# Performance work log

Measured on AMD Instinct MI355X. Metric: run time of the kernel, lower is better.

Reference implementation:

```python
import jax, jax.numpy as jnp
import numpy as np

B, X, Y, Z, C = 1, 16, 16, 16, 768
NUM_HEADS = 12


def setup_inputs() -> dict:
    key = jax.random.key(0)
    k0, k1, k2 = jax.random.split(key, 3)
    x = jax.random.normal(k0, (B, X, Y, Z, C), dtype=jnp.float32)
    # Linear weights stored as [in, out] (torch stores [out, in]; math is x @ W_in_out + b)
    w_qkv = jax.random.normal(k1, (C, 3 * C), dtype=jnp.float32) * 0.02
    b_qkv = jnp.zeros((3 * C,), dtype=jnp.float32)
    w_proj = jax.random.normal(k2, (C, C), dtype=jnp.float32) * 0.02
    b_proj = jnp.zeros((C,), dtype=jnp.float32)
    return {"x": x, "w_qkv": w_qkv, "b_qkv": b_qkv, "w_proj": w_proj, "b_proj": b_proj}


def reference(x, w_qkv, b_qkv, w_proj, b_proj):
    b, xx, yy, zz, c = x.shape
    h = NUM_HEADS
    hd = c // h
    scale = hd ** (-0.5)
    n = xx * yy * zz  # flatten 3D grid into tokens

    qkv = x.reshape(b, n, c) @ w_qkv + b_qkv          # [B, N, 3C]
    qkv = qkv.reshape(b, n, 3, h, hd).transpose(2, 0, 3, 1, 4)  # [3, B, H, N, hd]
    q, k, v = qkv[0], qkv[1], qkv[2]

    attn = jnp.einsum('bhnd,bhmd->bhnm', q * scale, k)  # [B, H, N, N]
    attn = jax.nn.softmax(attn, axis=-1)
    out = jnp.einsum('bhnm,bhmd->bhnd', attn, v)        # [B, H, N, hd]
    out = out.transpose(0, 2, 1, 3).reshape(b, n, c)
    out = out @ w_proj + b_proj
    return out.reshape(b, xx, yy, zz, c)
```

## Files before the change

### kernel.cpp

```cpp
#include <hip/hip_runtime.h>
#include <cstddef>

#define N_TOK 4096
#define C_DIM 768
#define H_NUM 12
#define C3    2304
#define NSPLIT 4

typedef unsigned short u16;
using short8  = __attribute__((ext_vector_type(8))) short;
using floatx4 = __attribute__((ext_vector_type(4))) float;
using u16x4   = __attribute__((ext_vector_type(4))) u16;
using uint4v  = __attribute__((ext_vector_type(4))) unsigned;

#define K2SCALE 0.18033688011112043f

__device__ __forceinline__ u16 f2bf(float f) {
  union { float f; unsigned u; } v; v.f = f;
  unsigned r = v.u + 0x7FFFu + ((v.u >> 16) & 1u);
  return (u16)(r >> 16);
}

__device__ __forceinline__ unsigned permpack(float a, float b) {
  union { float f; unsigned u; } x, y; x.f = a; y.f = b;
  return __builtin_amdgcn_perm(y.u, x.u, 0x07060302u);
}

__device__ __forceinline__ float aexp2(float x) {
  float r;
  asm("v_exp_f32 %0, %1" : "=v"(r) : "v"(x));
  return r;
}

__device__ __forceinline__ float arcp(float x) {
  float r;
  asm("v_rcp_f32 %0, %1" : "=v"(r) : "v"(x));
  return r;
}

__device__ __forceinline__ void pl_swap32(unsigned &a, unsigned &b) {
#if __has_builtin(__builtin_amdgcn_permlane32_swap)
  auto r = __builtin_amdgcn_permlane32_swap(a, b, false, false);
  a = r[0]; b = r[1];
#else
  asm("v_permlane32_swap_b32 %0, %1" : "+v"(a), "+v"(b));
#endif
}
__device__ __forceinline__ void pl_swap16(unsigned &a, unsigned &b) {
#if __has_builtin(__builtin_amdgcn_permlane16_swap)
  auto r = __builtin_amdgcn_permlane16_swap(a, b, false, false);
  a = r[0]; b = r[1];
#else
  asm("v_permlane16_swap_b32 %0, %1" : "+v"(a), "+v"(b));
#endif
}

__device__ __forceinline__ void gload_lds16(const void* g, void* l) {
  __builtin_amdgcn_global_load_lds(
      (const __attribute__((address_space(1))) unsigned int*)g,
      (__attribute__((address_space(3))) unsigned int*)l, 16, 0, 0);
}

__global__ void k_pre(const float* __restrict__ x, u16* __restrict__ xb,
                      const float* __restrict__ wq, u16* __restrict__ wqT,
                      const float* __restrict__ wp, u16* __restrict__ wpT,
                      float* __restrict__ Oz) {
  __shared__ float tile[32][33];
  const int b = blockIdx.x;
  if (b >= 5376) {
    size_t i = (size_t)(b - 5376) * 256 + threadIdx.x;
    float4 z; z.x = 0.f; z.y = 0.f; z.z = 0.f; z.w = 0.f;
    ((float4*)Oz)[i] = z;
    return;
  }
  if (b < 3072) {
    int i = b * 256 + threadIdx.x;
    float4 f = ((const float4*)x)[i];
    u16x4 o;
    o[0] = f2bf(f.x); o[1] = f2bf(f.y); o[2] = f2bf(f.z); o[3] = f2bf(f.w);
    ((u16x4*)xb)[i] = o;
    return;
  }
  const float* in; u16* out; int Cc, bx, by;
  if (b < 4800) { int t = b - 3072; in = wq; out = wqT; Cc = 2304; bx = t % 72; by = t / 72; }
  else          { int t = b - 4800; in = wp; out = wpT; Cc = 768;  bx = t % 24; by = t / 24; }
  const int R = 768;
  const int tx = threadIdx.x & 31;
  const int ty = threadIdx.x >> 5;
  const int c0 = bx * 32, r0 = by * 32;
#pragma unroll
  for (int i = 0; i < 32; i += 8)
    tile[ty + i][tx] = in[(size_t)(r0 + ty + i) * Cc + c0 + tx];
  __syncthreads();
#pragma unroll
  for (int i = 0; i < 32; i += 8)
    out[(size_t)(c0 + ty + i) * R + r0 + tx] = f2bf(tile[tx][ty + i]);
}

template <int MODE>
__global__ __launch_bounds__(256)
void k_gemm_bt(const u16* __restrict__ A, const u16* __restrict__ B,
               const float* __restrict__ bias, void* __restrict__ outp,
               u16* __restrict__ vT, int K) {
  __shared__ u16 As[128 * 32];
  __shared__ u16 Bs[128 * 32];
  const int tid  = threadIdx.x;
  const int wave = tid >> 6, lane = tid & 63, quad = lane >> 4, l16 = lane & 15;
  const int wrow = wave >> 1, wcol = wave & 1;
  const int bm = blockIdx.y, bn = blockIdx.x;
  const int r3 = l16 & 3;

  floatx4 acc[4][4];
#pragma unroll
  for (int i = 0; i < 4; ++i)
#pragma unroll
    for (int j = 0; j < 4; ++j)
#pragma unroll
      for (int r = 0; r < 4; ++r) acc[i][j][r] = 0.f;

  const int ar = tid >> 2;
  const int ac = ((tid & 3) ^ (ar & 3)) * 8;
  const u16* gA = A + (size_t)(bm * 128 + ar) * K + ac;
  const u16* gB = B + (size_t)(bn * 128 + ar) * K + ac;
  u16* lA = &As[0] + tid * 8;
  u16* lB = &Bs[0] + tid * 8;

  for (int k0 = 0; k0 < K; k0 += 32) {
    gload_lds16(gA + k0,                  lA);
    gload_lds16(gA + k0 + (size_t)64 * K, lA + 2048);
    gload_lds16(gB + k0,                  lB);
    gload_lds16(gB + k0 + (size_t)64 * K, lB + 2048);
    __syncthreads();
    short8 af[4], bf[4];
#pragma unroll
    for (int t = 0; t < 4; ++t) {
      af[t] = *(const short8*)&As[(wrow * 64 + t * 16 + l16) * 32 + ((quad ^ r3) * 8)];
      bf[t] = *(const short8*)&Bs[(wcol * 64 + t * 16 + l16) * 32 + ((quad ^ r3) * 8)];
    }
#pragma unroll
    for (int tm = 0; tm < 4; ++tm)
#pragma unroll
      for (int tn = 0; tn < 4; ++tn)
        acc[tm][tn] = __builtin_amdgcn_mfma_f32_16x16x32_bf16(af[tm], bf[tn], acc[tm][tn], 0, 0, 0);
    __syncthreads();
  }

  if (MODE == 0) {
    u16* qkv = (u16*)outp;
    const float qs = (bn < 6) ? K2SCALE : 1.0f;
#pragma unroll
    for (int tn = 0; tn < 4; ++tn) {
      const int col = bn * 128 + wcol * 64 + tn * 16 + l16;
      const float bc = bias[col];
      if (col < 1536) {
#pragma unroll
        for (int tm = 0; tm < 4; ++tm) {
          const int rowb = bm * 128 + wrow * 64 + tm * 16 + quad * 4;
#pragma unroll
          for (int r = 0; r < 4; ++r)
            qkv[(size_t)(rowb + r) * C3 + col] = f2bf((acc[tm][tn][r] + bc) * qs);
        }
      } else {
        const int hd_ = col - 1536;
#pragma unroll
        for (int tm = 0; tm < 4; ++tm) {
          const int rowb = bm * 128 + wrow * 64 + tm * 16 + quad * 4;
          u16x4 pk;
#pragma unroll
          for (int r = 0; r < 4; ++r) pk[r] = f2bf(acc[tm][tn][r] + bc);
          *(u16x4*)&vT[(size_t)hd_ * N_TOK + rowb] = pk;
        }
      }
    }
  } else {
    float* out = (float*)outp;
#pragma unroll
    for (int tn = 0; tn < 4; ++tn) {
      const int col = bn * 128 + wcol * 64 + tn * 16 + l16;
      const float bc = bias[col];
#pragma unroll
      for (int tm = 0; tm < 4; ++tm) {
        const int rowb = bm * 128 + wrow * 64 + tm * 16 + quad * 4;
#pragma unroll
        for (int r = 0; r < 4; ++r)
          out[(size_t)(rowb + r) * C_DIM + col] = acc[tm][tn][r] + bc;
      }
    }
  }
}

__global__ __launch_bounds__(256, 4)
void k_flash(const u16* __restrict__ qkv, const u16* __restrict__ vT,
             float* __restrict__ Opart, float* __restrict__ lpart) {
  __shared__ u16 Ks[2][64 * 64];
  __shared__ u16 Vs[2][64 * 64];
  const int tid  = threadIdx.x;
  const int wave = tid >> 6, lane = tid & 63, quad = lane >> 4, l16 = lane & 15;
  const int qt = blockIdx.x, h = blockIdx.y, split = blockIdx.z;
  const int lr = tid >> 3;
  const int lc = ((tid & 7) ^ (lr & 7)) * 8;
  const int r7 = l16 & 7;
  const int kb = split * 1024;

  short8 bq[2][2];
#pragma unroll
  for (int qs = 0; qs < 2; ++qs)
#pragma unroll
    for (int ks = 0; ks < 2; ++ks)
      bq[qs][ks] = *(const short8*)&qkv[(size_t)(qt * 128 + wave * 32 + qs * 16 + l16) * C3
                                        + h * 64 + ks * 32 + quad * 8];

  const u16* gk = qkv + (size_t)lr * C3 + C_DIM + h * 64 + lc;
  const u16* gv = vT + (size_t)(h * 64 + lr) * N_TOK + lc;

  auto stage = [&](int b, int m0) {
#pragma unroll
    for (int p = 0; p < 2; ++p) {
      gload_lds16(gk + (size_t)(m0 + p * 32) * C3,    &Ks[b][p * 2048 + tid * 8]);
      gload_lds16(gv + (size_t)(p * 32) * N_TOK + m0, &Vs[b][p * 2048 + tid * 8]);
    }
  };

  floatx4 o0[4], o1[4], l0, l1, zv;
#pragma unroll
  for (int r = 0; r < 4; ++r) { zv[r] = 0.f; l0[r] = 0.f; l1[r] = 0.f; }
#pragma unroll
  for (int d = 0; d < 4; ++d)
#pragma unroll
    for (int r = 0; r < 4; ++r) { o0[d][r] = 0.f; o1[d][r] = 0.f; }

  short8 ones;
#pragma unroll
  for (int i = 0; i < 8; ++i) ones[i] = (short)0x3F80;

  auto compute = [&](int b) __attribute__((always_inline)) {
    const u16* kbp = &Ks[b][0];
    const u16* vb  = &Vs[b][0];
    floatx4 s0[4], s1[4];
    __builtin_amdgcn_s_setprio(1);
#pragma unroll
    for (int tn = 0; tn < 4; ++tn) {
      short8 ak = *(const short8*)&kbp[(tn * 16 + l16) * 64 + (quad ^ r7) * 8];
      s0[tn] = __builtin_amdgcn_mfma_f32_16x16x32_bf16(ak, bq[0][0], zv, 0, 0, 0);
      s1[tn] = __builtin_amdgcn_mfma_f32_16x16x32_bf16(ak, bq[1][0], zv, 0, 0, 0);
    }
#pragma unroll
    for (int tn = 0; tn < 4; ++tn) {
      short8 ak = *(const short8*)&kbp[(tn * 16 + l16) * 64 + ((quad + 4) ^ r7) * 8];
      s0[tn] = __builtin_amdgcn_mfma_f32_16x16x32_bf16(ak, bq[0][1], s0[tn], 0, 0, 0);
      s1[tn] = __builtin_amdgcn_mfma_f32_16x16x32_bf16(ak, bq[1][1], s1[tn], 0, 0, 0);
    }
    __builtin_amdgcn_s_setprio(0);

    unsigned pk0[4][2], pk1[4][2];
#pragma unroll
    for (int tn = 0; tn < 4; ++tn) {
      pk0[tn][0] = permpack(aexp2(s0[tn][0]), aexp2(s0[tn][1]));
      pk0[tn][1] = permpack(aexp2(s0[tn][2]), aexp2(s0[tn][3]));
      pk1[tn][0] = permpack(aexp2(s1[tn][0]), aexp2(s1[tn][1]));
      pk1[tn][1] = permpack(aexp2(s1[tn][2]), aexp2(s1[tn][3]));
    }
#pragma unroll
    for (int t1 = 0; t1 < 2; ++t1)
#pragma unroll
      for (int w = 0; w < 2; ++w) {
        pl_swap32(pk0[2 * t1][w], pk0[2 * t1 + 1][w]);
        pl_swap16(pk0[2 * t1][w], pk0[2 * t1 + 1][w]);
        pl_swap32(pk1[2 * t1][w], pk1[2 * t1 + 1][w]);
        pl_swap16(pk1[2 * t1][w], pk1[2 * t1 + 1][w]);
      }

#pragma unroll
    for (int ks = 0; ks < 2; ++ks) {
      uint4v t0v, t1v;
      t0v[0] = pk0[2 * ks][0]; t0v[1] = pk0[2 * ks][1];
      t0v[2] = pk0[2 * ks + 1][0]; t0v[3] = pk0[2 * ks + 1][1];
      t1v[0] = pk1[2 * ks][0]; t1v[1] = pk1[2 * ks][1];
      t1v[2] = pk1[2 * ks + 1][0]; t1v[3] = pk1[2 * ks + 1][1];
      const short8 ap0 = __builtin_bit_cast(short8, t0v);
      const short8 ap1 = __builtin_bit_cast(short8, t1v);
      __builtin_amdgcn_s_setprio(1);
#pragma unroll
      for (int dt = 0; dt < 4; ++dt) {
        short8 bv = *(const short8*)&vb[(dt * 16 + l16) * 64 + ((quad + 4 * ks) ^ r7) * 8];
        o0[dt] = __builtin_amdgcn_mfma_f32_16x16x32_bf16(ap0, bv, o0[dt], 0, 0, 0);
        o1[dt] = __builtin_amdgcn_mfma_f32_16x16x32_bf16(ap1, bv, o1[dt], 0, 0, 0);
      }
      l0 = __builtin_amdgcn_mfma_f32_16x16x32_bf16(ap0, ones, l0, 0, 0, 0);
      l1 = __builtin_amdgcn_mfma_f32_16x16x32_bf16(ap1, ones, l1, 0, 0, 0);
      __builtin_amdgcn_s_setprio(0);
    }
  };

  stage(0, kb);
  __syncthreads();
  int m0 = kb + 64;
  for (int it2 = 0; it2 < 7; ++it2) {
    stage(1, m0); m0 += 64;
    compute(0);
    __syncthreads();
    stage(0, m0); m0 += 64;
    compute(1);
    __syncthreads();
  }
  stage(1, m0);
  compute(0);
  __syncthreads();
  compute(1);

  const int rowg = qt * 128 + wave * 32 + quad * 4;
  float* Ob = Opart + (size_t)h * N_TOK * 64;
  float* lb = lpart + (size_t)h * N_TOK;
#pragma unroll
  for (int r = 0; r < 4; ++r) {
#pragma unroll
    for (int dt = 0; dt < 4; ++dt) {
      const int col = dt * 16 + l16;
      atomicAdd(&Ob[(size_t)(rowg + r) * 64 + col],      o0[dt][r]);
      atomicAdd(&Ob[(size_t)(rowg + 16 + r) * 64 + col], o1[dt][r]);
    }
    if (l16 == 0) {
      atomicAdd(&lb[rowg + r],      l0[r]);
      atomicAdd(&lb[rowg + 16 + r], l1[r]);
    }
  }
}

__global__ void k_combine(const float* __restrict__ Op, const float* __restrict__ lp,
                          u16* __restrict__ ao) {
  const int idx = blockIdx.x * 256 + threadIdx.x;
  const int col = idx & 63;
  const int row = idx >> 6;
  const float o = Op[(size_t)row * 64 + col];
  const float l = lp[row];
  const int h = row >> 12, q = row & 4095;
  ao[(size_t)q * C_DIM + h * 64 + col] = f2bf(o * arcp(l));
}

extern "C" void kernel_launch(void* const* d_in, const int* in_sizes, int n_in,
                              void* d_out, int out_size, void* d_ws, size_t ws_size,
                              hipStream_t stream) {
  const float* x      = (const float*)d_in[0];
  const float* w_qkv  = (const float*)d_in[1];
  const float* b_qkv  = (const float*)d_in[2];
  const float* w_proj = (const float*)d_in[3];
  const float* b_proj = (const float*)d_in[4];
  float* out = (float*)d_out;

  u16* xb     = (u16*)d_ws;
  u16* wqkvT  = xb     + (size_t)N_TOK * C_DIM;
  u16* wprojT = wqkvT  + (size_t)C3 * C_DIM;
  u16* qkv    = wprojT + (size_t)C_DIM * C_DIM;
  u16* vT     = qkv    + (size_t)N_TOK * C3;
  u16* ao     = vT     + (size_t)C_DIM * N_TOK;
  float* Opart = (float*)(ao + (size_t)N_TOK * C_DIM);
  float* lpart = Opart + (size_t)H_NUM * N_TOK * 64;

  k_pre<<<8496, 256, 0, stream>>>(x, xb, w_qkv, wqkvT, w_proj, wprojT, Opart);
  k_gemm_bt<0><<<dim3(C3 / 128, N_TOK / 128), 256, 0, stream>>>(xb, wqkvT, b_qkv, qkv, vT, C_DIM);
  k_flash<<<dim3(N_TOK / 128, H_NUM, NSPLIT), 256, 0, stream>>>(qkv, vT, Opart, lpart);
  k_combine<<<H_NUM * N_TOK * 64 / 256, 256, 0, stream>>>(Opart, lpart, ao);
  k_gemm_bt<1><<<dim3(C_DIM / 128, N_TOK / 128), 256, 0, stream>>>(ao, wprojT, b_proj, out, nullptr, C_DIM);
}
```

Before: 203.7 us.

## Load V fragments directly from global memory and double the key split count

V tiles are no longer staged through shared memory. Each wave now reads its V^T fragments straight from global memory (and L2) inside the compute step, which halves the LDS footprint and allows an occupancy hint of 5 blocks. NSPLIT goes from 4 to 8, so each block handles 512 keys and the grid has twice as many blocks. The trade-off is more global-load latency in the inner loop, with no prefetch of V, plus twice as many atomic partial-output reductions.

```diff
diff --git a/kernel.cpp b/kernel.cpp
--- a/kernel.cpp
+++ b/kernel.cpp
@@ -5,7 +5,7 @@
 #define C_DIM 768
 #define H_NUM 12
 #define C3    2304
-#define NSPLIT 4
+#define NSPLIT 8
 
 typedef unsigned short u16;
 using short8  = __attribute__((ext_vector_type(8))) short;
@@ -189,18 +189,17 @@
   }
 }
 
-__global__ __launch_bounds__(256, 4)
+__global__ __launch_bounds__(256, 5)
 void k_flash(const u16* __restrict__ qkv, const u16* __restrict__ vT,
              float* __restrict__ Opart, float* __restrict__ lpart) {
   __shared__ u16 Ks[2][64 * 64];
-  __shared__ u16 Vs[2][64 * 64];
   const int tid  = threadIdx.x;
   const int wave = tid >> 6, lane = tid & 63, quad = lane >> 4, l16 = lane & 15;
   const int qt = blockIdx.x, h = blockIdx.y, split = blockIdx.z;
   const int lr = tid >> 3;
   const int lc = ((tid & 7) ^ (lr & 7)) * 8;
   const int r7 = l16 & 7;
-  const int kb = split * 1024;
+  const int kb = split * (N_TOK / NSPLIT);
 
   short8 bq[2][2];
 #pragma unroll
@@ -211,14 +210,12 @@
                                         + h * 64 + ks * 32 + quad * 8];
 
   const u16* gk = qkv + (size_t)lr * C3 + C_DIM + h * 64 + lc;
-  const u16* gv = vT + (size_t)(h * 64 + lr) * N_TOK + lc;
+  const u16* gv = vT + (size_t)(h * 64 + l16) * N_TOK + quad * 8;
 
   auto stage = [&](int b, int m0) {
 #pragma unroll
-    for (int p = 0; p < 2; ++p) {
-      gload_lds16(gk + (size_t)(m0 + p * 32) * C3,    &Ks[b][p * 2048 + tid * 8]);
-      gload_lds16(gv + (size_t)(p * 32) * N_TOK + m0, &Vs[b][p * 2048 + tid * 8]);
-    }
+    for (int p = 0; p < 2; ++p)
+      gload_lds16(gk + (size_t)(m0 + p * 32) * C3, &Ks[b][p * 2048 + tid * 8]);
   };
 
   floatx4 o0[4], o1[4], l0, l1, zv;
@@ -233,9 +230,8 @@
 #pragma unroll
   for (int i = 0; i < 8; ++i) ones[i] = (short)0x3F80;
 
-  auto compute = [&](int b) __attribute__((always_inline)) {
+  auto compute = [&](int b, int m0) __attribute__((always_inline)) {
     const u16* kbp = &Ks[b][0];
-    const u16* vb  = &Vs[b][0];
     floatx4 s0[4], s1[4];
     __builtin_amdgcn_s_setprio(1);
 #pragma unroll
@@ -279,12 +275,15 @@
       t1v[2] = pk1[2 * ks + 1][0]; t1v[3] = pk1[2 * ks + 1][1];
       const short8 ap0 = __builtin_bit_cast(short8, t0v);
       const short8 ap1 = __builtin_bit_cast(short8, t1v);
+      short8 bv[4];
+#pragma unroll
+      for (int dt = 0; dt < 4; ++dt)
+        bv[dt] = *(const short8*)&gv[(size_t)(dt * 16) * N_TOK + m0 + 4 * ks * 8];
       __builtin_amdgcn_s_setprio(1);
 #pragma unroll
       for (int dt = 0; dt < 4; ++dt) {
-        short8 bv = *(const short8*)&vb[(dt * 16 + l16) * 64 + ((quad + 4 * ks) ^ r7) * 8];
-        o0[dt] = __builtin_amdgcn_mfma_f32_16x16x32_bf16(ap0, bv, o0[dt], 0, 0, 0);
-        o1[dt] = __builtin_amdgcn_mfma_f32_16x16x32_bf16(ap1, bv, o1[dt], 0, 0, 0);
+        o0[dt] = __builtin_amdgcn_mfma_f32_16x16x32_bf16(ap0, bv[dt], o0[dt], 0, 0, 0);
+        o1[dt] = __builtin_amdgcn_mfma_f32_16x16x32_bf16(ap1, bv[dt], o1[dt], 0, 0, 0);
       }
       l0 = __builtin_amdgcn_mfma_f32_16x16x32_bf16(ap0, ones, l0, 0, 0, 0);
       l1 = __builtin_amdgcn_mfma_f32_16x16x32_bf16(ap1, ones, l1, 0, 0, 0);
@@ -295,18 +294,18 @@
   stage(0, kb);
   __syncthreads();
   int m0 = kb + 64;
-  for (int it2 = 0; it2 < 7; ++it2) {
-    stage(1, m0); m0 += 64;
-    compute(0);
+  for (int it2 = 0; it2 < 3; ++it2) {
+    stage(1, m0);
+    compute(0, m0 - 64); m0 += 64;
     __syncthreads();
-    stage(0, m0); m0 += 64;
-    compute(1);
+    stage(0, m0);
+    compute(1, m0 - 64); m0 += 64;
     __syncthreads();
   }
   stage(1, m0);
-  compute(0);
+  compute(0, m0 - 64);
   __syncthreads();
-  compute(1);
+  compute(1, m0);
 
   const int rowg = qt * 128 + wave * 32 + quad * 4;
   float* Ob = Opart + (size_t)h * N_TOK * 64;
```

Result: slower. 361.5 us (+77.4%).
